# Kernel optimization log

Measured on AMD Instinct MI355X. Metric: run time of the kernel, lower is better.

The kernel has to match this reference:

```python
import jax, jax.numpy as jnp
import numpy as np

N_NODES = 60000
IN_CH = 128
HID = 32
ACT_DIM = 6
N_EDGES = 600000


def setup_inputs() -> dict:
    key = jax.random.key(0)
    ks = jax.random.split(key, 10)
    state = jax.random.normal(ks[0], (N_NODES, IN_CH), dtype=jnp.float32)
    edge_index = jax.random.randint(ks[1], (2, N_EDGES), 0, N_NODES, dtype=jnp.int64)
    s_g = 1.0 / np.sqrt(IN_CH)
    s_h = 1.0 / np.sqrt(HID)
    Wg = jax.random.uniform(ks[2], (IN_CH, IN_CH), jnp.float32, -s_g, s_g)
    bg = jax.random.uniform(ks[3], (IN_CH,), jnp.float32, -s_g, s_g)
    W1 = jax.random.uniform(ks[4], (IN_CH, HID), jnp.float32, -s_g, s_g)
    b1 = jax.random.uniform(ks[5], (HID,), jnp.float32, -s_g, s_g)
    W2 = jax.random.uniform(ks[6], (HID, HID), jnp.float32, -s_h, s_h)
    b2 = jax.random.uniform(ks[7], (HID,), jnp.float32, -s_h, s_h)
    W3 = jax.random.uniform(ks[8], (HID, 1), jnp.float32, -s_h, s_h)
    b3 = jax.random.uniform(ks[9], (1,), jnp.float32, -s_h, s_h)
    return {"state": state, "Wg": Wg, "bg": bg, "W1": W1, "b1": b1,
            "W2": W2, "b2": b2, "W3": W3, "b3": b3, "edge_index": edge_index}


def reference(state, Wg, bg, W1, b1, W2, b2, W3, b3, edge_index):
    N = state.shape[0]
    # GCNConv: add self-loops, symmetric degree normalization
    loop = jnp.arange(N, dtype=edge_index.dtype)
    src = jnp.concatenate([edge_index[0], loop])
    dst = jnp.concatenate([edge_index[1], loop])
    deg = jax.ops.segment_sum(jnp.ones_like(dst, dtype=state.dtype), dst, num_segments=N)
    dinv = jax.lax.rsqrt(deg)  # deg >= 1 thanks to self-loops
    norm = dinv[src] * dinv[dst]  # [E+N]
    h = state @ Wg  # [N, C]
    agg = jax.ops.segment_sum(h[src] * norm[:, None], dst, num_segments=N) + bg
    out = jax.nn.relu(agg)
    x = (out + state).reshape(-1, ACT_DIM, IN_CH)  # [B, 6, C]
    x = jax.nn.leaky_relu(x @ W1 + b1)
    x = jax.nn.leaky_relu(x @ W2 + b2)
    conc = jax.nn.softplus(x @ W3 + b3)[..., 0]  # [B, 6]
    # deterministic, mode==0
    action = conc / (conc.sum() + 1e-20)
    return action
```

## Files before the change

### kernel.cpp

```cpp
#include <hip/hip_runtime.h>
#include <hip/hip_bf16.h>
#include <math.h>

#define N_NODES 60000
#define IN_CH   128
#define HID     32
#define N_EDGES 600000
#define CAP     32

#define WS_CNT    0
#define WS_SUM    60000
#define WS_BUCKET 60008
#define WS_HS     2940032
#define WS_X      10620032

typedef float  v4f __attribute__((ext_vector_type(4)));
typedef short  v8s __attribute__((ext_vector_type(8)));

static __device__ inline short f2bf(float f) {
    __hip_bfloat16 h = __float2bfloat16(f);
    union { __hip_bfloat16 h; short s; } u; u.h = h; return u.s;
}
static __device__ inline float bf2f(short s) {
    return __uint_as_float(((unsigned int)(unsigned short)s) << 16);
}
static __device__ inline float bflo(unsigned int u) { return __uint_as_float(u << 16); }
static __device__ inline float bfhi(unsigned int u) { return __uint_as_float(u & 0xffff0000u); }
static __device__ inline int   rdl_i(int v, int l)   { return __builtin_amdgcn_readlane(v, l); }
static __device__ inline float rdl_f(float v, int l) {
    return __int_as_float(__builtin_amdgcn_readlane(__float_as_int(v), l));
}

__launch_bounds__(256)
__global__ void k_fat(const float* __restrict__ state, const float* __restrict__ Wg,
                      const int* __restrict__ eidx, int* __restrict__ cnt,
                      int* __restrict__ bucket, unsigned short* __restrict__ hs) {
    __shared__ __align__(16) short Bs[128 * 136];
    const int bid = blockIdx.x;
    const int r7 = bid % 7, q7 = bid / 7;
    const int t = threadIdx.x;

    if (r7 >= 2) {
        const int hb = q7 * 5 + (r7 - 2);
        const int i = hb * 256 + t;
        if (i < N_EDGES) {
            int s = eidx[i];
            int d = eidx[N_EDGES + i];
            int slot = atomicAdd(&cnt[d], 1);
            if (slot < CAP) bucket[d * CAP + slot] = s;
        }
        return;
    }

    const int gb = q7 * 2 + r7;

    for (int idx = t; idx < 128 * 128; idx += 256) {
        int k = idx >> 7, n = idx & 127;
        Bs[n * 136 + k] = f2bf(Wg[idx]);
    }
    __syncthreads();

    const int w = t >> 6, lane = t & 63;
    const int quad = lane >> 4, m = lane & 15;
    const int rowBase = gb * 64;
    int arow = rowBase + w * 16 + m;
    if (arow > N_NODES - 1) arow = N_NODES - 1;

    v8s a[4];
    const float4* sp = (const float4*)(state + (size_t)arow * 128);
#pragma unroll
    for (int q = 0; q < 4; ++q) {
        float4 v0 = sp[q * 8 + quad * 2];
        float4 v1 = sp[q * 8 + quad * 2 + 1];
        v8s af;
        af[0] = f2bf(v0.x); af[1] = f2bf(v0.y); af[2] = f2bf(v0.z); af[3] = f2bf(v0.w);
        af[4] = f2bf(v1.x); af[5] = f2bf(v1.y); af[6] = f2bf(v1.z); af[7] = f2bf(v1.w);
        a[q] = af;
    }

    v4f acc[8];
#pragma unroll
    for (int tt = 0; tt < 8; ++tt) acc[tt] = (v4f)0.f;

#pragma unroll
    for (int tt = 0; tt < 8; ++tt) {
        const short* bp = &Bs[(tt * 16 + m) * 136];
#pragma unroll
        for (int q = 0; q < 4; ++q) {
            v8s b = *(const v8s*)(bp + q * 32 + quad * 8);
            acc[tt] = __builtin_amdgcn_mfma_f32_16x16x32_bf16(a[q], b, acc[tt], 0, 0, 0);
        }
    }

#pragma unroll
    for (int tt = 0; tt < 8; ++tt) {
#pragma unroll
        for (int r = 0; r < 4; ++r) {
            int rr = rowBase + w * 16 + quad * 4 + r;
            if (rr < N_NODES)
                hs[(size_t)rr * 128 + tt * 16 + m] = (unsigned short)f2bf(acc[tt][r]);
        }
    }
}

__launch_bounds__(256)
__global__ void k_gather(const unsigned short* __restrict__ hs, const float* __restrict__ state,
                         const int* __restrict__ cnt, const int* __restrict__ bucket,
                         const float* __restrict__ bg, unsigned int* __restrict__ xb) {
    const int wave = threadIdx.x >> 6, lane = threadIdx.x & 63;
    const int row = blockIdx.x * 4 + wave;
    if (row >= N_NODES) return;
    const int ci = cnt[row];
    const float dinv = rsqrtf((float)ci + 1.0f);
    const int nb = ci < CAP ? ci : CAP;

    int slot = 0; float dv = 0.f;
    if (lane < nb) {
        slot = bucket[row * CAP + lane];
        dv = rsqrtf((float)cnt[slot] + 1.0f);
    }

    const unsigned int* hp = (const unsigned int*)hs;
    float ax, ay;
    {
        unsigned int u = hp[(unsigned)row * 64u + lane];
        ax = bflo(u) * dinv;
        ay = bfhi(u) * dinv;
    }
    int s = 0;
    for (; s + 8 <= nb; s += 8) {
        int   s0 = rdl_i(slot, s + 0), s1 = rdl_i(slot, s + 1);
        int   s2 = rdl_i(slot, s + 2), s3 = rdl_i(slot, s + 3);
        int   s4 = rdl_i(slot, s + 4), s5 = rdl_i(slot, s + 5);
        int   s6 = rdl_i(slot, s + 6), s7 = rdl_i(slot, s + 7);
        float d0 = rdl_f(dv, s + 0), d1 = rdl_f(dv, s + 1);
        float d2 = rdl_f(dv, s + 2), d3 = rdl_f(dv, s + 3);
        float d4 = rdl_f(dv, s + 4), d5 = rdl_f(dv, s + 5);
        float d6 = rdl_f(dv, s + 6), d7 = rdl_f(dv, s + 7);
        unsigned int u0 = hp[(unsigned)s0 * 64u + lane];
        unsigned int u1 = hp[(unsigned)s1 * 64u + lane];
        unsigned int u2 = hp[(unsigned)s2 * 64u + lane];
        unsigned int u3 = hp[(unsigned)s3 * 64u + lane];
        unsigned int u4 = hp[(unsigned)s4 * 64u + lane];
        unsigned int u5 = hp[(unsigned)s5 * 64u + lane];
        unsigned int u6 = hp[(unsigned)s6 * 64u + lane];
        unsigned int u7 = hp[(unsigned)s7 * 64u + lane];
        ax = fmaf(d0, bflo(u0), ax); ay = fmaf(d0, bfhi(u0), ay);
        ax = fmaf(d1, bflo(u1), ax); ay = fmaf(d1, bfhi(u1), ay);
        ax = fmaf(d2, bflo(u2), ax); ay = fmaf(d2, bfhi(u2), ay);
        ax = fmaf(d3, bflo(u3), ax); ay = fmaf(d3, bfhi(u3), ay);
        ax = fmaf(d4, bflo(u4), ax); ay = fmaf(d4, bfhi(u4), ay);
        ax = fmaf(d5, bflo(u5), ax); ay = fmaf(d5, bfhi(u5), ay);
        ax = fmaf(d6, bflo(u6), ax); ay = fmaf(d6, bfhi(u6), ay);
        ax = fmaf(d7, bflo(u7), ax); ay = fmaf(d7, bfhi(u7), ay);
    }
    for (; s + 4 <= nb; s += 4) {
        int   s0 = rdl_i(slot, s + 0), s1 = rdl_i(slot, s + 1);
        int   s2 = rdl_i(slot, s + 2), s3 = rdl_i(slot, s + 3);
        float d0 = rdl_f(dv, s + 0), d1 = rdl_f(dv, s + 1);
        float d2 = rdl_f(dv, s + 2), d3 = rdl_f(dv, s + 3);
        unsigned int u0 = hp[(unsigned)s0 * 64u + lane];
        unsigned int u1 = hp[(unsigned)s1 * 64u + lane];
        unsigned int u2 = hp[(unsigned)s2 * 64u + lane];
        unsigned int u3 = hp[(unsigned)s3 * 64u + lane];
        ax = fmaf(d0, bflo(u0), ax); ay = fmaf(d0, bfhi(u0), ay);
        ax = fmaf(d1, bflo(u1), ax); ay = fmaf(d1, bfhi(u1), ay);
        ax = fmaf(d2, bflo(u2), ax); ay = fmaf(d2, bfhi(u2), ay);
        ax = fmaf(d3, bflo(u3), ax); ay = fmaf(d3, bfhi(u3), ay);
    }
    for (; s < nb; ++s) {
        int   s0 = rdl_i(slot, s);
        float d0 = rdl_f(dv, s);
        unsigned int u = hp[(unsigned)s0 * 64u + lane];
        ax = fmaf(d0, bflo(u), ax);
        ay = fmaf(d0, bfhi(u), ay);
    }
    float2 bgv = ((const float2*)bg)[lane];
    float2 st  = ((const float2*)state)[(unsigned)row * 64u + lane];
    float ox = fmaxf(fmaf(dinv, ax, bgv.x), 0.f) + st.x;
    float oy = fmaxf(fmaf(dinv, ay, bgv.y), 0.f) + st.y;
    unsigned int pack = ((unsigned int)(unsigned short)f2bf(oy) << 16)
                      | ((unsigned int)(unsigned short)f2bf(ox));
    xb[(unsigned)row * 64u + lane] = pack;
}

__launch_bounds__(256)
__global__ void k_mlp(const unsigned int* __restrict__ xb,
                      const float* __restrict__ W1, const float* __restrict__ b1,
                      const float* __restrict__ W2, const float* __restrict__ b2,
                      const float* __restrict__ W3, const float* __restrict__ b3,
                      float* __restrict__ out, float* __restrict__ sum) {
    __shared__ __align__(16) short BsH[32 * 136];
    __shared__ __align__(16) short BsL[32 * 136];
    __shared__ float  zs[4][16 * 33];
    __shared__ float4 W2s[32 * 8];
    __shared__ float  b1s[32], b2s[32], W3s[32];
    __shared__ float  wred[4];
    const int t = threadIdx.x;

    for (int idx = t; idx < 128 * 32; idx += 256) {
        int k = idx >> 5, j = idx & 31;
        float f = W1[idx];
        short hi = f2bf(f);
        short lo = f2bf(f - bf2f(hi));
        BsH[j * 136 + k] = hi;
        BsL[j * 136 + k] = lo;
    }
    W2s[t] = ((const float4*)W2)[t];
    if (t < 32) { b1s[t] = b1[t]; b2s[t] = b2[t]; W3s[t] = W3[t]; }
    __syncthreads();

    const int wv = t >> 6, lane = t & 63;
    const int quad = lane >> 4, m = lane & 15;
    const int rbase = (blockIdx.x * 4 + wv) * 16;
    float wavesum = 0.f;

    if (rbase < N_NODES) {
        v8s a[4];
        const int4* xp = (const int4*)(xb + (size_t)(rbase + m) * 64);
#pragma unroll
        for (int q = 0; q < 4; ++q) a[q] = *(const v8s*)&xp[q * 4 + quad];

        v4f acc0 = (v4f)0.f, acc1 = (v4f)0.f;
#pragma unroll
        for (int q = 0; q < 4; ++q) {
            v8s bh0 = *(const v8s*)&BsH[m * 136 + q * 32 + quad * 8];
            v8s bh1 = *(const v8s*)&BsH[(16 + m) * 136 + q * 32 + quad * 8];
            acc0 = __builtin_amdgcn_mfma_f32_16x16x32_bf16(a[q], bh0, acc0, 0, 0, 0);
            acc1 = __builtin_amdgcn_mfma_f32_16x16x32_bf16(a[q], bh1, acc1, 0, 0, 0);
        }
#pragma unroll
        for (int q = 0; q < 4; ++q) {
            v8s bl0 = *(const v8s*)&BsL[m * 136 + q * 32 + quad * 8];
            v8s bl1 = *(const v8s*)&BsL[(16 + m) * 136 + q * 32 + quad * 8];
            acc0 = __builtin_amdgcn_mfma_f32_16x16x32_bf16(a[q], bl0, acc0, 0, 0, 0);
            acc1 = __builtin_amdgcn_mfma_f32_16x16x32_bf16(a[q], bl1, acc1, 0, 0, 0);
        }

        float bj0 = b1s[m], bj1 = b1s[16 + m];
#pragma unroll
        for (int r = 0; r < 4; ++r) {
            float h0 = acc0[r] + bj0; h0 = h0 > 0.f ? h0 : 0.01f * h0;
            float h1 = acc1[r] + bj1; h1 = h1 > 0.f ? h1 : 0.01f * h1;
            zs[wv][(quad * 4 + r) * 33 + m]      = h0;
            zs[wv][(quad * 4 + r) * 33 + 16 + m] = h1;
        }
        asm volatile("s_waitcnt lgkmcnt(0)" ::: "memory");

        float h2[8];
#pragma unroll
        for (int j = 0; j < 8; ++j) h2[j] = b2s[quad * 8 + j];
        const float* zrow = &zs[wv][m * 33];
#pragma unroll
        for (int k = 0; k < 32; ++k) {
            float zk = zrow[k];
            float4 wA = W2s[k * 8 + quad * 2];
            float4 wB = W2s[k * 8 + quad * 2 + 1];
            h2[0] = fmaf(zk, wA.x, h2[0]); h2[1] = fmaf(zk, wA.y, h2[1]);
            h2[2] = fmaf(zk, wA.z, h2[2]); h2[3] = fmaf(zk, wA.w, h2[3]);
            h2[4] = fmaf(zk, wB.x, h2[4]); h2[5] = fmaf(zk, wB.y, h2[5]);
            h2[6] = fmaf(zk, wB.z, h2[6]); h2[7] = fmaf(zk, wB.w, h2[7]);
        }
        float a3p = 0.f;
#pragma unroll
        for (int j = 0; j < 8; ++j) {
            float z2 = h2[j] > 0.f ? h2[j] : 0.01f * h2[j];
            a3p = fmaf(z2, W3s[quad * 8 + j], a3p);
        }
        a3p += __shfl_xor(a3p, 16, 64);
        a3p += __shfl_xor(a3p, 32, 64);
        float a3 = a3p + b3[0];
        float sp = fmaxf(a3, 0.f) + log1pf(expf(-fabsf(a3)));
        if (quad == 0) out[rbase + m] = sp;
        float p = (quad == 0) ? sp : 0.f;
#pragma unroll
        for (int off = 32; off >= 1; off >>= 1) p += __shfl_xor(p, off, 64);
        wavesum = p;
    }
    if (lane == 0) wred[wv] = wavesum;
    __syncthreads();
    if (t == 0) atomicAdd(sum, (wred[0] + wred[1]) + (wred[2] + wred[3]));
}

__global__ void k_norm(const float* __restrict__ sum, float* __restrict__ out) {
    int i = blockIdx.x * blockDim.x + threadIdx.x;
    if (i < N_NODES / 4) {
        float inv = 1.0f / (*sum + 1e-20f);
        float4* o4 = (float4*)out;
        float4 v = o4[i];
        v.x *= inv; v.y *= inv; v.z *= inv; v.w *= inv;
        o4[i] = v;
    }
}

extern "C" void kernel_launch(void* const* d_in, const int* in_sizes, int n_in,
                              void* d_out, int out_size, void* d_ws, size_t ws_size,
                              hipStream_t stream) {
    const float* state = (const float*)d_in[0];
    const float* Wg    = (const float*)d_in[1];
    const float* bg    = (const float*)d_in[2];
    const float* W1    = (const float*)d_in[3];
    const float* b1    = (const float*)d_in[4];
    const float* W2    = (const float*)d_in[5];
    const float* b2    = (const float*)d_in[6];
    const float* W3    = (const float*)d_in[7];
    const float* b3    = (const float*)d_in[8];
    const int*   eidx  = (const int*)d_in[9];
    float* out = (float*)d_out;

    int*   wi = (int*)d_ws;
    float* wf = (float*)d_ws;
    int*   cnt    = wi + WS_CNT;
    float* sum    = wf + WS_SUM;
    int*   bucket = wi + WS_BUCKET;
    unsigned short* hs = (unsigned short*)(wf + WS_HS);
    unsigned int*   xb = (unsigned int*)(wf + WS_X);

    hipMemsetAsync(cnt, 0, 60001 * sizeof(int), stream);

    k_fat<<<3282, 256, 0, stream>>>(state, Wg, eidx, cnt, bucket, hs);
    k_gather<<<(N_NODES + 3) / 4, 256, 0, stream>>>(hs, state, cnt, bucket, bg, xb);
    k_mlp<<<938, 256, 0, stream>>>(xb, W1, b1, W2, b2, W3, b3, out, sum);
    k_norm<<<(N_NODES / 4 + 255) / 256, 256, 0, stream>>>(sum, out);
}
```

Baseline: 177.4 us.

## Fuse neighbor gather into MLP kernel and slice edge bucketing by destination range

The separate gather kernel is folded into the MLP kernel. Each wave aggregates its 16 rows and writes the packed bf16 result to shared memory instead of a global intermediate, which removes a kernel launch and the global write and read of the activation buffer. Edge bucketing is reorganised so the GEMM blocks come first and histogram blocks follow. Each edge is now read by 8 blocks, and each of those blocks only handles destinations in its own 7500-node slice, which is meant to localise the atomics. The price is that edge destinations are read 8 times, and the gather now runs on only 938 blocks of 4 waves each, which lowers the parallelism available for hiding latency.

```diff
diff --git a/kernel.cpp b/kernel.cpp
--- a/kernel.cpp
+++ b/kernel.cpp
@@ -12,7 +12,10 @@
 #define WS_SUM    60000
 #define WS_BUCKET 60008
 #define WS_HS     2940032
-#define WS_X      10620032
+
+#define GEMM_BLOCKS 938
+#define HIST_BLOCKS 18752
+#define SLICE_SZ    7500
 
 typedef float  v4f __attribute__((ext_vector_type(4)));
 typedef short  v8s __attribute__((ext_vector_type(8)));
@@ -37,22 +40,26 @@
                       int* __restrict__ bucket, unsigned short* __restrict__ hs) {
     __shared__ __align__(16) short Bs[128 * 136];
     const int bid = blockIdx.x;
-    const int r7 = bid % 7, q7 = bid / 7;
     const int t = threadIdx.x;
 
-    if (r7 >= 2) {
-        const int hb = q7 * 5 + (r7 - 2);
-        const int i = hb * 256 + t;
-        if (i < N_EDGES) {
-            int s = eidx[i];
-            int d = eidx[N_EDGES + i];
-            int slot = atomicAdd(&cnt[d], 1);
-            if (slot < CAP) bucket[d * CAP + slot] = s;
+    if (bid >= GEMM_BLOCKS) {
+        const int u = bid - GEMM_BLOCKS;
+        const int c = u >> 3;
+        const int s = bid & 7;
+        const int lo = s * SLICE_SZ;
+        const int e = c * 256 + t;
+        if (e < N_EDGES) {
+            int d = eidx[N_EDGES + e];
+            if ((unsigned)(d - lo) < (unsigned)SLICE_SZ) {
+                int sv = eidx[e];
+                int slot = atomicAdd(&cnt[d], 1);
+                if (slot < CAP) bucket[d * CAP + slot] = sv;
+            }
         }
         return;
     }
 
-    const int gb = q7 * 2 + r7;
+    const int gb = bid;
 
     for (int idx = t; idx < 128 * 128; idx += 256) {
         int k = idx >> 7, n = idx & 127;
@@ -104,96 +111,18 @@
 }
 
 __launch_bounds__(256)
-__global__ void k_gather(const unsigned short* __restrict__ hs, const float* __restrict__ state,
-                         const int* __restrict__ cnt, const int* __restrict__ bucket,
-                         const float* __restrict__ bg, unsigned int* __restrict__ xb) {
-    const int wave = threadIdx.x >> 6, lane = threadIdx.x & 63;
-    const int row = blockIdx.x * 4 + wave;
-    if (row >= N_NODES) return;
-    const int ci = cnt[row];
-    const float dinv = rsqrtf((float)ci + 1.0f);
-    const int nb = ci < CAP ? ci : CAP;
-
-    int slot = 0; float dv = 0.f;
-    if (lane < nb) {
-        slot = bucket[row * CAP + lane];
-        dv = rsqrtf((float)cnt[slot] + 1.0f);
-    }
-
-    const unsigned int* hp = (const unsigned int*)hs;
-    float ax, ay;
-    {
-        unsigned int u = hp[(unsigned)row * 64u + lane];
-        ax = bflo(u) * dinv;
-        ay = bfhi(u) * dinv;
-    }
-    int s = 0;
-    for (; s + 8 <= nb; s += 8) {
-        int   s0 = rdl_i(slot, s + 0), s1 = rdl_i(slot, s + 1);
-        int   s2 = rdl_i(slot, s + 2), s3 = rdl_i(slot, s + 3);
-        int   s4 = rdl_i(slot, s + 4), s5 = rdl_i(slot, s + 5);
-        int   s6 = rdl_i(slot, s + 6), s7 = rdl_i(slot, s + 7);
-        float d0 = rdl_f(dv, s + 0), d1 = rdl_f(dv, s + 1);
-        float d2 = rdl_f(dv, s + 2), d3 = rdl_f(dv, s + 3);
-        float d4 = rdl_f(dv, s + 4), d5 = rdl_f(dv, s + 5);
-        float d6 = rdl_f(dv, s + 6), d7 = rdl_f(dv, s + 7);
-        unsigned int u0 = hp[(unsigned)s0 * 64u + lane];
-        unsigned int u1 = hp[(unsigned)s1 * 64u + lane];
-        unsigned int u2 = hp[(unsigned)s2 * 64u + lane];
-        unsigned int u3 = hp[(unsigned)s3 * 64u + lane];
-        unsigned int u4 = hp[(unsigned)s4 * 64u + lane];
-        unsigned int u5 = hp[(unsigned)s5 * 64u + lane];
-        unsigned int u6 = hp[(unsigned)s6 * 64u + lane];
-        unsigned int u7 = hp[(unsigned)s7 * 64u + lane];
-        ax = fmaf(d0, bflo(u0), ax); ay = fmaf(d0, bfhi(u0), ay);
-        ax = fmaf(d1, bflo(u1), ax); ay = fmaf(d1, bfhi(u1), ay);
-        ax = fmaf(d2, bflo(u2), ax); ay = fmaf(d2, bfhi(u2), ay);
-        ax = fmaf(d3, bflo(u3), ax); ay = fmaf(d3, bfhi(u3), ay);
-        ax = fmaf(d4, bflo(u4), ax); ay = fmaf(d4, bfhi(u4), ay);
-        ax = fmaf(d5, bflo(u5), ax); ay = fmaf(d5, bfhi(u5), ay);
-        ax = fmaf(d6, bflo(u6), ax); ay = fmaf(d6, bfhi(u6), ay);
-        ax = fmaf(d7, bflo(u7), ax); ay = fmaf(d7, bfhi(u7), ay);
-    }
-    for (; s + 4 <= nb; s += 4) {
-        int   s0 = rdl_i(slot, s + 0), s1 = rdl_i(slot, s + 1);
-        int   s2 = rdl_i(slot, s + 2), s3 = rdl_i(slot, s + 3);
-        float d0 = rdl_f(dv, s + 0), d1 = rdl_f(dv, s + 1);
-        float d2 = rdl_f(dv, s + 2), d3 = rdl_f(dv, s + 3);
-        unsigned int u0 = hp[(unsigned)s0 * 64u + lane];
-        unsigned int u1 = hp[(unsigned)s1 * 64u + lane];
-        unsigned int u2 = hp[(unsigned)s2 * 64u + lane];
-        unsigned int u3 = hp[(unsigned)s3 * 64u + lane];
-        ax = fmaf(d0, bflo(u0), ax); ay = fmaf(d0, bfhi(u0), ay);
-        ax = fmaf(d1, bflo(u1), ax); ay = fmaf(d1, bfhi(u1), ay);
-        ax = fmaf(d2, bflo(u2), ax); ay = fmaf(d2, bfhi(u2), ay);
-        ax = fmaf(d3, bflo(u3), ax); ay = fmaf(d3, bfhi(u3), ay);
-    }
-    for (; s < nb; ++s) {
-        int   s0 = rdl_i(slot, s);
-        float d0 = rdl_f(dv, s);
-        unsigned int u = hp[(unsigned)s0 * 64u + lane];
-        ax = fmaf(d0, bflo(u), ax);
-        ay = fmaf(d0, bfhi(u), ay);
-    }
-    float2 bgv = ((const float2*)bg)[lane];
-    float2 st  = ((const float2*)state)[(unsigned)row * 64u + lane];
-    float ox = fmaxf(fmaf(dinv, ax, bgv.x), 0.f) + st.x;
-    float oy = fmaxf(fmaf(dinv, ay, bgv.y), 0.f) + st.y;
-    unsigned int pack = ((unsigned int)(unsigned short)f2bf(oy) << 16)
-                      | ((unsigned int)(unsigned short)f2bf(ox));
-    xb[(unsigned)row * 64u + lane] = pack;
-}
-
-__launch_bounds__(256)
-__global__ void k_mlp(const unsigned int* __restrict__ xb,
-                      const float* __restrict__ W1, const float* __restrict__ b1,
-                      const float* __restrict__ W2, const float* __restrict__ b2,
-                      const float* __restrict__ W3, const float* __restrict__ b3,
-                      float* __restrict__ out, float* __restrict__ sum) {
+__global__ void k_gm(const unsigned short* __restrict__ hs, const float* __restrict__ state,
+                     const int* __restrict__ cnt, const int* __restrict__ bucket,
+                     const float* __restrict__ bg,
+                     const float* __restrict__ W1, const float* __restrict__ b1,
+                     const float* __restrict__ W2, const float* __restrict__ b2,
+                     const float* __restrict__ W3, const float* __restrict__ b3,
+                     float* __restrict__ out, float* __restrict__ sum) {
     __shared__ __align__(16) short BsH[32 * 136];
     __shared__ __align__(16) short BsL[32 * 136];
-    __shared__ float  zs[4][16 * 33];
+    __shared__ __align__(16) unsigned int xz[4][16 * 68];
     __shared__ float4 W2s[32 * 8];
+    __shared__ float  bgs[128];
     __shared__ float  b1s[32], b2s[32], W3s[32];
     __shared__ float  wred[4];
     const int t = threadIdx.x;
@@ -207,6 +136,7 @@
         BsL[j * 136 + k] = lo;
     }
     W2s[t] = ((const float4*)W2)[t];
+    if (t < 128) bgs[t] = bg[t];
     if (t < 32) { b1s[t] = b1[t]; b2s[t] = b2[t]; W3s[t] = W3[t]; }
     __syncthreads();
 
@@ -216,10 +146,87 @@
     float wavesum = 0.f;
 
     if (rbase < N_NODES) {
+        const unsigned int* hp = (const unsigned int*)hs;
+        float bgx = bgs[2 * lane], bgy = bgs[2 * lane + 1];
+
+        for (int i = 0; i < 16; ++i) {
+            const int row = rbase + i;
+            const int ci = cnt[row];
+            const float dinv = rsqrtf((float)ci + 1.0f);
+            const int nb = ci < CAP ? ci : CAP;
+            int slot = 0; float dv = 0.f;
+            if (lane < nb) {
+                slot = bucket[row * CAP + lane];
+                dv = rsqrtf((float)cnt[slot] + 1.0f);
+            }
+            float ax, ay;
+            {
+                unsigned int u = hp[(unsigned)row * 64u + lane];
+                ax = bflo(u) * dinv;
+                ay = bfhi(u) * dinv;
+            }
+            int s = 0;
+            for (; s + 8 <= nb; s += 8) {
+                int   s0 = rdl_i(slot, s + 0), s1 = rdl_i(slot, s + 1);
+                int   s2 = rdl_i(slot, s + 2), s3 = rdl_i(slot, s + 3);
+                int   s4 = rdl_i(slot, s + 4), s5 = rdl_i(slot, s + 5);
+                int   s6 = rdl_i(slot, s + 6), s7 = rdl_i(slot, s + 7);
+                float d0 = rdl_f(dv, s + 0), d1 = rdl_f(dv, s + 1);
+                float d2 = rdl_f(dv, s + 2), d3 = rdl_f(dv, s + 3);
+                float d4 = rdl_f(dv, s + 4), d5 = rdl_f(dv, s + 5);
+                float d6 = rdl_f(dv, s + 6), d7 = rdl_f(dv, s + 7);
+                unsigned int u0 = hp[(unsigned)s0 * 64u + lane];
+                unsigned int u1 = hp[(unsigned)s1 * 64u + lane];
+                unsigned int u2 = hp[(unsigned)s2 * 64u + lane];
+                unsigned int u3 = hp[(unsigned)s3 * 64u + lane];
+                unsigned int u4 = hp[(unsigned)s4 * 64u + lane];
+                unsigned int u5 = hp[(unsigned)s5 * 64u + lane];
+                unsigned int u6 = hp[(unsigned)s6 * 64u + lane];
+                unsigned int u7 = hp[(unsigned)s7 * 64u + lane];
+                ax = fmaf(d0, bflo(u0), ax); ay = fmaf(d0, bfhi(u0), ay);
+                ax = fmaf(d1, bflo(u1), ax); ay = fmaf(d1, bfhi(u1), ay);
+                ax = fmaf(d2, bflo(u2), ax); ay = fmaf(d2, bfhi(u2), ay);
+                ax = fmaf(d3, bflo(u3), ax); ay = fmaf(d3, bfhi(u3), ay);
+                ax = fmaf(d4, bflo(u4), ax); ay = fmaf(d4, bfhi(u4), ay);
+                ax = fmaf(d5, bflo(u5), ax); ay = fmaf(d5, bfhi(u5), ay);
+                ax = fmaf(d6, bflo(u6), ax); ay = fmaf(d6, bfhi(u6), ay);
+                ax = fmaf(d7, bflo(u7), ax); ay = fmaf(d7, bfhi(u7), ay);
+            }
+            for (; s + 4 <= nb; s += 4) {
+                int   s0 = rdl_i(slot, s + 0), s1 = rdl_i(slot, s + 1);
+                int   s2 = rdl_i(slot, s + 2), s3 = rdl_i(slot, s + 3);
+                float d0 = rdl_f(dv, s + 0), d1 = rdl_f(dv, s + 1);
+                float d2 = rdl_f(dv, s + 2), d3 = rdl_f(dv, s + 3);
+                unsigned int u0 = hp[(unsigned)s0 * 64u + lane];
+                unsigned int u1 = hp[(unsigned)s1 * 64u + lane];
+                unsigned int u2 = hp[(unsigned)s2 * 64u + lane];
+                unsigned int u3 = hp[(unsigned)s3 * 64u + lane];
+                ax = fmaf(d0, bflo(u0), ax); ay = fmaf(d0, bfhi(u0), ay);
+                ax = fmaf(d1, bflo(u1), ax); ay = fmaf(d1, bfhi(u1), ay);
+                ax = fmaf(d2, bflo(u2), ax); ay = fmaf(d2, bfhi(u2), ay);
+                ax = fmaf(d3, bflo(u3), ax); ay = fmaf(d3, bfhi(u3), ay);
+            }
+            for (; s < nb; ++s) {
+                int   s0 = rdl_i(slot, s);
+                float d0 = rdl_f(dv, s);
+                unsigned int u = hp[(unsigned)s0 * 64u + lane];
+                ax = fmaf(d0, bflo(u), ax);
+                ay = fmaf(d0, bfhi(u), ay);
+            }
+            float2 st = ((const float2*)state)[(unsigned)row * 64u + lane];
+            float ox = fmaxf(fmaf(dinv, ax, bgx), 0.f) + st.x;
+            float oy = fmaxf(fmaf(dinv, ay, bgy), 0.f) + st.y;
+            unsigned int pack = ((unsigned int)(unsigned short)f2bf(oy) << 16)
+                              | ((unsigned int)(unsigned short)f2bf(ox));
+            xz[wv][i * 68 + lane] = pack;
+        }
+        asm volatile("s_waitcnt lgkmcnt(0)" ::: "memory");
+
         v8s a[4];
-        const int4* xp = (const int4*)(xb + (size_t)(rbase + m) * 64);
-#pragma unroll
-        for (int q = 0; q < 4; ++q) a[q] = *(const v8s*)&xp[q * 4 + quad];
+#pragma unroll
+        for (int q = 0; q < 4; ++q)
+            a[q] = *(const v8s*)&xz[wv][m * 68 + q * 16 + quad * 4];
+        asm volatile("s_waitcnt lgkmcnt(0)" ::: "memory");
 
         v4f acc0 = (v4f)0.f, acc1 = (v4f)0.f;
 #pragma unroll
@@ -237,20 +244,21 @@
             acc1 = __builtin_amdgcn_mfma_f32_16x16x32_bf16(a[q], bl1, acc1, 0, 0, 0);
         }
 
+        float* zs = (float*)&xz[wv][0];
         float bj0 = b1s[m], bj1 = b1s[16 + m];
 #pragma unroll
         for (int r = 0; r < 4; ++r) {
             float h0 = acc0[r] + bj0; h0 = h0 > 0.f ? h0 : 0.01f * h0;
             float h1 = acc1[r] + bj1; h1 = h1 > 0.f ? h1 : 0.01f * h1;
-            zs[wv][(quad * 4 + r) * 33 + m]      = h0;
-            zs[wv][(quad * 4 + r) * 33 + 16 + m] = h1;
+            zs[(quad * 4 + r) * 33 + m]      = h0;
+            zs[(quad * 4 + r) * 33 + 16 + m] = h1;
         }
         asm volatile("s_waitcnt lgkmcnt(0)" ::: "memory");
 
         float h2[8];
 #pragma unroll
         for (int j = 0; j < 8; ++j) h2[j] = b2s[quad * 8 + j];
-        const float* zrow = &zs[wv][m * 33];
+        const float* zrow = &zs[m * 33];
 #pragma unroll
         for (int k = 0; k < 32; ++k) {
             float zk = zrow[k];
@@ -314,12 +322,11 @@
     float* sum    = wf + WS_SUM;
     int*   bucket = wi + WS_BUCKET;
     unsigned short* hs = (unsigned short*)(wf + WS_HS);
-    unsigned int*   xb = (unsigned int*)(wf + WS_X);
 
     hipMemsetAsync(cnt, 0, 60001 * sizeof(int), stream);
 
-    k_fat<<<3282, 256, 0, stream>>>(state, Wg, eidx, cnt, bucket, hs);
-    k_gather<<<(N_NODES + 3) / 4, 256, 0, stream>>>(hs, state, cnt, bucket, bg, xb);
-    k_mlp<<<938, 256, 0, stream>>>(xb, W1, b1, W2, b2, W3, b3, out, sum);
+    k_fat<<<GEMM_BLOCKS + HIST_BLOCKS, 256, 0, stream>>>(state, Wg, eidx, cnt, bucket, hs);
+    k_gm<<<938, 256, 0, stream>>>(hs, state, cnt, bucket, bg,
+                                  W1, b1, W2, b2, W3, b3, out, sum);
     k_norm<<<(N_NODES / 4 + 255) / 256, 256, 0, stream>>>(sum, out);
 }
```

New measurement: 221.5 us. 24.9% more time.

## Split histogram from GEMM and pre-scale GEMM rows by source dinv

Applied to the files above, without the earlier changes.

The fused histogram+GEMM kernel is split into two kernels, so the GEMM can read the final degree counts and store h rows already multiplied by each node's inverse sqrt degree. The gather kernel then no longer loads cnt per neighbor or computes rsqrt for it; it just sums bf16 rows. This removes a dependent random load per edge from the gather, but adds a kernel launch and serializes the histogram before the GEMM, losing the overlap the fused kernel had.

```diff
diff --git a/kernel.cpp b/kernel.cpp
--- a/kernel.cpp
+++ b/kernel.cpp
@@ -26,33 +26,23 @@
 }
 static __device__ inline float bflo(unsigned int u) { return __uint_as_float(u << 16); }
 static __device__ inline float bfhi(unsigned int u) { return __uint_as_float(u & 0xffff0000u); }
-static __device__ inline int   rdl_i(int v, int l)   { return __builtin_amdgcn_readlane(v, l); }
-static __device__ inline float rdl_f(float v, int l) {
-    return __int_as_float(__builtin_amdgcn_readlane(__float_as_int(v), l));
+static __device__ inline int rdl_i(int v, int l) { return __builtin_amdgcn_readlane(v, l); }
+
+__global__ void k_hist(const int* __restrict__ eidx, int* __restrict__ cnt,
+                       int* __restrict__ bucket) {
+    int i = blockIdx.x * blockDim.x + threadIdx.x;
+    if (i >= N_EDGES) return;
+    int s = eidx[i];
+    int d = eidx[N_EDGES + i];
+    int slot = atomicAdd(&cnt[d], 1);
+    if (slot < CAP) bucket[d * CAP + slot] = s;
 }
 
 __launch_bounds__(256)
-__global__ void k_fat(const float* __restrict__ state, const float* __restrict__ Wg,
-                      const int* __restrict__ eidx, int* __restrict__ cnt,
-                      int* __restrict__ bucket, unsigned short* __restrict__ hs) {
+__global__ void k_gemm(const float* __restrict__ state, const float* __restrict__ Wg,
+                       const int* __restrict__ cnt, unsigned short* __restrict__ hs) {
     __shared__ __align__(16) short Bs[128 * 136];
-    const int bid = blockIdx.x;
-    const int r7 = bid % 7, q7 = bid / 7;
     const int t = threadIdx.x;
-
-    if (r7 >= 2) {
-        const int hb = q7 * 5 + (r7 - 2);
-        const int i = hb * 256 + t;
-        if (i < N_EDGES) {
-            int s = eidx[i];
-            int d = eidx[N_EDGES + i];
-            int slot = atomicAdd(&cnt[d], 1);
-            if (slot < CAP) bucket[d * CAP + slot] = s;
-        }
-        return;
-    }
-
-    const int gb = q7 * 2 + r7;
 
     for (int idx = t; idx < 128 * 128; idx += 256) {
         int k = idx >> 7, n = idx & 127;
@@ -62,7 +52,7 @@
 
     const int w = t >> 6, lane = t & 63;
     const int quad = lane >> 4, m = lane & 15;
-    const int rowBase = gb * 64;
+    const int rowBase = blockIdx.x * 64;
     int arow = rowBase + w * 16 + m;
     if (arow > N_NODES - 1) arow = N_NODES - 1;
 
@@ -92,13 +82,19 @@
         }
     }
 
+    float dinv[4];
+#pragma unroll
+    for (int r = 0; r < 4; ++r) {
+        int rr = rowBase + w * 16 + quad * 4 + r;
+        dinv[r] = (rr < N_NODES) ? rsqrtf((float)cnt[rr] + 1.0f) : 0.f;
+    }
 #pragma unroll
     for (int tt = 0; tt < 8; ++tt) {
 #pragma unroll
         for (int r = 0; r < 4; ++r) {
             int rr = rowBase + w * 16 + quad * 4 + r;
             if (rr < N_NODES)
-                hs[(size_t)rr * 128 + tt * 16 + m] = (unsigned short)f2bf(acc[tt][r]);
+                hs[(size_t)rr * 128 + tt * 16 + m] = (unsigned short)f2bf(acc[tt][r] * dinv[r]);
         }
     }
 }
@@ -114,29 +110,21 @@
     const float dinv = rsqrtf((float)ci + 1.0f);
     const int nb = ci < CAP ? ci : CAP;
 
-    int slot = 0; float dv = 0.f;
-    if (lane < nb) {
-        slot = bucket[row * CAP + lane];
-        dv = rsqrtf((float)cnt[slot] + 1.0f);
-    }
+    int slot = (lane < nb) ? bucket[row * CAP + lane] : 0;
 
     const unsigned int* hp = (const unsigned int*)hs;
     float ax, ay;
     {
         unsigned int u = hp[(unsigned)row * 64u + lane];
-        ax = bflo(u) * dinv;
-        ay = bfhi(u) * dinv;
+        ax = bflo(u);
+        ay = bfhi(u);
     }
     int s = 0;
     for (; s + 8 <= nb; s += 8) {
-        int   s0 = rdl_i(slot, s + 0), s1 = rdl_i(slot, s + 1);
-        int   s2 = rdl_i(slot, s + 2), s3 = rdl_i(slot, s + 3);
-        int   s4 = rdl_i(slot, s + 4), s5 = rdl_i(slot, s + 5);
-        int   s6 = rdl_i(slot, s + 6), s7 = rdl_i(slot, s + 7);
-        float d0 = rdl_f(dv, s + 0), d1 = rdl_f(dv, s + 1);
-        float d2 = rdl_f(dv, s + 2), d3 = rdl_f(dv, s + 3);
-        float d4 = rdl_f(dv, s + 4), d5 = rdl_f(dv, s + 5);
-        float d6 = rdl_f(dv, s + 6), d7 = rdl_f(dv, s + 7);
+        int s0 = rdl_i(slot, s + 0), s1 = rdl_i(slot, s + 1);
+        int s2 = rdl_i(slot, s + 2), s3 = rdl_i(slot, s + 3);
+        int s4 = rdl_i(slot, s + 4), s5 = rdl_i(slot, s + 5);
+        int s6 = rdl_i(slot, s + 6), s7 = rdl_i(slot, s + 7);
         unsigned int u0 = hp[(unsigned)s0 * 64u + lane];
         unsigned int u1 = hp[(unsigned)s1 * 64u + lane];
         unsigned int u2 = hp[(unsigned)s2 * 64u + lane];
@@ -145,35 +133,26 @@
         unsigned int u5 = hp[(unsigned)s5 * 64u + lane];
         unsigned int u6 = hp[(unsigned)s6 * 64u + lane];
         unsigned int u7 = hp[(unsigned)s7 * 64u + lane];
-        ax = fmaf(d0, bflo(u0), ax); ay = fmaf(d0, bfhi(u0), ay);
-        ax = fmaf(d1, bflo(u1), ax); ay = fmaf(d1, bfhi(u1), ay);
-        ax = fmaf(d2, bflo(u2), ax); ay = fmaf(d2, bfhi(u2), ay);
-        ax = fmaf(d3, bflo(u3), ax); ay = fmaf(d3, bfhi(u3), ay);
-        ax = fmaf(d4, bflo(u4), ax); ay = fmaf(d4, bfhi(u4), ay);
-        ax = fmaf(d5, bflo(u5), ax); ay = fmaf(d5, bfhi(u5), ay);
-        ax = fmaf(d6, bflo(u6), ax); ay = fmaf(d6, bfhi(u6), ay);
-        ax = fmaf(d7, bflo(u7), ax); ay = fmaf(d7, bfhi(u7), ay);
+        ax += bflo(u0) + bflo(u1) + bflo(u2) + bflo(u3)
+            + bflo(u4) + bflo(u5) + bflo(u6) + bflo(u7);
+        ay += bfhi(u0) + bfhi(u1) + bfhi(u2) + bfhi(u3)
+            + bfhi(u4) + bfhi(u5) + bfhi(u6) + bfhi(u7);
     }
     for (; s + 4 <= nb; s += 4) {
-        int   s0 = rdl_i(slot, s + 0), s1 = rdl_i(slot, s + 1);
-        int   s2 = rdl_i(slot, s + 2), s3 = rdl_i(slot, s + 3);
-        float d0 = rdl_f(dv, s + 0), d1 = rdl_f(dv, s + 1);
-        float d2 = rdl_f(dv, s + 2), d3 = rdl_f(dv, s + 3);
+        int s0 = rdl_i(slot, s + 0), s1 = rdl_i(slot, s + 1);
+        int s2 = rdl_i(slot, s + 2), s3 = rdl_i(slot, s + 3);
         unsigned int u0 = hp[(unsigned)s0 * 64u + lane];
         unsigned int u1 = hp[(unsigned)s1 * 64u + lane];
         unsigned int u2 = hp[(unsigned)s2 * 64u + lane];
         unsigned int u3 = hp[(unsigned)s3 * 64u + lane];
-        ax = fmaf(d0, bflo(u0), ax); ay = fmaf(d0, bfhi(u0), ay);
-        ax = fmaf(d1, bflo(u1), ax); ay = fmaf(d1, bfhi(u1), ay);
-        ax = fmaf(d2, bflo(u2), ax); ay = fmaf(d2, bfhi(u2), ay);
-        ax = fmaf(d3, bflo(u3), ax); ay = fmaf(d3, bfhi(u3), ay);
+        ax += bflo(u0) + bflo(u1) + bflo(u2) + bflo(u3);
+        ay += bfhi(u0) + bfhi(u1) + bfhi(u2) + bfhi(u3);
     }
     for (; s < nb; ++s) {
-        int   s0 = rdl_i(slot, s);
-        float d0 = rdl_f(dv, s);
+        int s0 = rdl_i(slot, s);
         unsigned int u = hp[(unsigned)s0 * 64u + lane];
-        ax = fmaf(d0, bflo(u), ax);
-        ay = fmaf(d0, bfhi(u), ay);
+        ax += bflo(u);
+        ay += bfhi(u);
     }
     float2 bgv = ((const float2*)bg)[lane];
     float2 st  = ((const float2*)state)[(unsigned)row * 64u + lane];
@@ -318,7 +297,8 @@
 
     hipMemsetAsync(cnt, 0, 60001 * sizeof(int), stream);
 
-    k_fat<<<3282, 256, 0, stream>>>(state, Wg, eidx, cnt, bucket, hs);
+    k_hist<<<(N_EDGES + 255) / 256, 256, 0, stream>>>(eidx, cnt, bucket);
+    k_gemm<<<(N_NODES + 63) / 64, 256, 0, stream>>>(state, Wg, cnt, hs);
     k_gather<<<(N_NODES + 3) / 4, 256, 0, stream>>>(hs, state, cnt, bucket, bg, xb);
     k_mlp<<<938, 256, 0, stream>>>(xb, W1, b1, W2, b2, W3, b3, out, sum);
     k_norm<<<(N_NODES / 4 + 255) / 256, 256, 0, stream>>>(sum, out);
```

After: 180.6 us. Within noise of the previous version (+1.8%).
